# Kernel tuning notes

Measured on AMD Instinct MI355X. Metric: run time of the kernel, lower is better.

The kernel has to match this reference:

```python
import jax, jax.numpy as jnp
import numpy as np

N, E, F_IN, H0, H1, H2 = 50000, 800000, 128, 256, 256, 256
NEG = jnp.finfo(jnp.float32).min


def sage_max(x, src, dst, Wl, bl, Wr):
    # PyG SAGEConv(aggr='max'): lin_l(max_j x_j) + lin_r(x_i)
    agg = jax.ops.segment_max(x[src], dst, num_segments=N)  # [N, F]
    agg = jnp.where(agg <= NEG, 0.0, agg)  # isolated nodes -> 0
    return agg @ Wl + bl + x @ Wr


def setup_inputs() -> dict:
    key = jax.random.key(0)
    ks = jax.random.split(key, 16)
    g = lambda k, shp, fan: jax.random.normal(k, shp, jnp.float32) / np.sqrt(fan)
    inp = {
        "x": jax.random.normal(ks[0], (N, F_IN), jnp.float32),
        "edge_index": jax.random.randint(ks[1], (2, E), 0, N, jnp.int64),
        # shared_l1
        "Wl1": g(ks[2], (F_IN, H0), F_IN), "bl1": jnp.zeros((H0,), jnp.float32), "Wr1": g(ks[3], (F_IN, H0), F_IN),
        # shared_l2
        "Wl2": g(ks[4], (H0, H1), H0), "bl2": jnp.zeros((H1,), jnp.float32), "Wr2": g(ks[5], (H0, H1), H0),
        # rtang_l1 + head
        "Wla": g(ks[6], (H1, H2), H1), "bla": jnp.zeros((H2,), jnp.float32), "Wra": g(ks[7], (H1, H2), H1),
        "Wa": g(ks[8], (H2, 1), H2), "ba": jnp.zeros((1,), jnp.float32),
        # movedis_l1 + head
        "Wlm": g(ks[9], (H1, H2), H1), "blm": jnp.zeros((H2,), jnp.float32), "Wrm": g(ks[10], (H1, H2), H1),
        "Wm": g(ks[11], (H2, 1), H2), "bm": jnp.zeros((1,), jnp.float32),
    }
    return inp


def reference(x, edge_index, Wl1, bl1, Wr1, Wl2, bl2, Wr2,
              Wla, bla, Wra, Wa, ba, Wlm, blm, Wrm, Wm, bm):
    src, dst = edge_index[0], edge_index[1]
    h = jax.nn.relu(sage_max(x, src, dst, Wl1, bl1, Wr1))
    h = jax.nn.relu(sage_max(h, src, dst, Wl2, bl2, Wr2))
    rt = jax.nn.relu(sage_max(h, src, dst, Wla, bla, Wra))
    rt = (rt @ Wa + ba).reshape(-1)  # [N]
    mv = jax.nn.relu(sage_max(h, src, dst, Wlm, blm, Wrm))
    mv = (mv @ Wm + bm).reshape(-1)  # [N]
    return (rt, mv)
```

## Files before the change

kernel.cpp:

```cpp
#include <hip/hip_runtime.h>
#include <hip/hip_bf16.h>


#define NN 50000
#define NE 800000
#define HD 256
#define CAP 64

using bf16 = __hip_bfloat16;
typedef float f32x4 __attribute__((ext_vector_type(4)));
typedef short bf16x8 __attribute__((ext_vector_type(8)));

__device__ __forceinline__ void async16(const void* g, void* l) {
    __builtin_amdgcn_global_load_lds(
        (const __attribute__((address_space(1))) unsigned int*)g,
        (__attribute__((address_space(3))) unsigned int*)l, 16, 0, 0);
}

__device__ __forceinline__ unsigned short f2b(float f) {
    bf16 b = __float2bfloat16(f);
    return __builtin_bit_cast(unsigned short, b);
}

__global__ void k_scatter(const int* __restrict__ ei, int* __restrict__ cnt,
                          int* __restrict__ srcp) {
    int e = blockIdx.x * 256 + threadIdx.x;
    if (e < NE) {
        int d = ei[NE + e];
        int slot = atomicAdd(&cnt[d], 1);
        if (slot < CAP) srcp[(d << 6) + slot] = ei[e];
    }
}

__device__ __forceinline__ void pack1(const float* __restrict__ W,
                                      bf16* __restrict__ bt, int idx, int Ktot,
                                      int kofs) {
    int k = idx >> 8, n = idx & 255;
    bt[(size_t)n * Ktot + kofs + k] = __float2bfloat16(W[idx]);
}

#define PREP_CVT_B 6250
#define PREP_PACK_B 1792
#define PREP_CNT_B 196
#define PREP_B (PREP_CVT_B + PREP_PACK_B + PREP_CNT_B)

__global__ void k_prep(const float* __restrict__ x, bf16* __restrict__ xb,
                       const float* __restrict__ Wl1,
                       const float* __restrict__ Wr1,
                       const float* __restrict__ Wl2,
                       const float* __restrict__ Wr2,
                       const float* __restrict__ Wla,
                       const float* __restrict__ Wra,
                       const float* __restrict__ Wlm,
                       const float* __restrict__ Wrm, bf16* __restrict__ Bt1,
                       bf16* __restrict__ Bt2, bf16* __restrict__ Bta,
                       bf16* __restrict__ Btm, int* __restrict__ cnt) {
    int b = blockIdx.x;
    if (b < PREP_CVT_B) {
        int i = b * 256 + threadIdx.x;
        float4 v = ((const float4*)x)[i];
        ushort4 o;
        o.x = f2b(v.x); o.y = f2b(v.y); o.z = f2b(v.z); o.w = f2b(v.w);
        ((ushort4*)xb)[i] = o;
    } else if (b < PREP_CVT_B + PREP_PACK_B) {
        int idx = (b - PREP_CVT_B) * 256 + threadIdx.x;
        if (idx < 32768) pack1(Wl1, Bt1, idx, 256, 0);
        else if (idx < 65536) pack1(Wr1, Bt1, idx - 32768, 256, 128);
        else if (idx < 131072) pack1(Wl2, Bt2, idx - 65536, 512, 0);
        else if (idx < 196608) pack1(Wr2, Bt2, idx - 131072, 512, 256);
        else if (idx < 262144) pack1(Wla, Bta, idx - 196608, 512, 0);
        else if (idx < 327680) pack1(Wra, Bta, idx - 262144, 512, 256);
        else if (idx < 393216) pack1(Wlm, Btm, idx - 327680, 512, 0);
        else pack1(Wrm, Btm, idx - 393216, 512, 256);
    } else {
        int i = (b - PREP_CVT_B - PREP_PACK_B) * 256 + threadIdx.x;
        if (i < NN) cnt[i] = 0;
    }
}

template <int EPL>
__global__ __launch_bounds__(256) void k_agg(const bf16* __restrict__ feat,
                                             bf16* __restrict__ agg,
                                             const int* __restrict__ cnt,
                                             const int* __restrict__ srcp) {
    int node = blockIdx.x * 4 + (threadIdx.x >> 6);
    if (node >= NN) return;
    int lane = threadIdx.x & 63;
    int n = min(cnt[node], CAP);
    const int* __restrict__ lst = srcp + (node << 6);
    float m[EPL];
#pragma unroll
    for (int i = 0; i < EPL; ++i) m[i] = __int_as_float(0xff800000);

    auto acc2 = [&](unsigned v, int i0) {
        m[i0] = fmaxf(m[i0], __uint_as_float(v << 16));
        m[i0 + 1] = fmaxf(m[i0 + 1], __uint_as_float(v & 0xffff0000u));
    };

    int e = 0;
    for (; e + 7 < n; e += 8) {
        int s[8];
#pragma unroll
        for (int j = 0; j < 8; ++j) s[j] = lst[e + j];
        if (EPL == 2) {
            unsigned v[8];
#pragma unroll
            for (int j = 0; j < 8; ++j)
                v[j] = ((const unsigned*)feat)[(size_t)s[j] * 64 + lane];
#pragma unroll
            for (int j = 0; j < 8; ++j) acc2(v[j], 0);
        } else {
            uint2 v[8];
#pragma unroll
            for (int j = 0; j < 8; ++j)
                v[j] = ((const uint2*)feat)[(size_t)s[j] * 64 + lane];
#pragma unroll
            for (int j = 0; j < 8; ++j) { acc2(v[j].x, 0); acc2(v[j].y, 2); }
        }
    }
    for (; e + 3 < n; e += 4) {
        int s[4];
#pragma unroll
        for (int j = 0; j < 4; ++j) s[j] = lst[e + j];
        if (EPL == 2) {
            unsigned v[4];
#pragma unroll
            for (int j = 0; j < 4; ++j)
                v[j] = ((const unsigned*)feat)[(size_t)s[j] * 64 + lane];
#pragma unroll
            for (int j = 0; j < 4; ++j) acc2(v[j], 0);
        } else {
            uint2 v[4];
#pragma unroll
            for (int j = 0; j < 4; ++j)
                v[j] = ((const uint2*)feat)[(size_t)s[j] * 64 + lane];
#pragma unroll
            for (int j = 0; j < 4; ++j) { acc2(v[j].x, 0); acc2(v[j].y, 2); }
        }
    }
    for (; e < n; ++e) {
        int s = lst[e];
        if (EPL == 2) {
            acc2(((const unsigned*)feat)[(size_t)s * 64 + lane], 0);
        } else {
            uint2 v = ((const uint2*)feat)[(size_t)s * 64 + lane];
            acc2(v.x, 0); acc2(v.y, 2);
        }
    }
    unsigned r0 = 0, r1 = 0;
    if (n > 0) {
        r0 = (__float_as_uint(m[0]) >> 16) | (__float_as_uint(m[1]) & 0xffff0000u);
        if (EPL == 4)
            r1 = (__float_as_uint(m[2]) >> 16) | (__float_as_uint(m[3]) & 0xffff0000u);
    }
    if (EPL == 2) {
        ((unsigned*)agg)[(size_t)node * 64 + lane] = r0;
    } else {
        ((uint2*)agg)[(size_t)node * 64 + lane] = make_uint2(r0, r1);
    }
}

__device__ __forceinline__ void gemm_core256(const bf16* __restrict__ A0,
                                             const bf16* __restrict__ A1, int F,
                                             int Ktot,
                                             const bf16* __restrict__ Bt,
                                             int bm0, int t, short* As,
                                             short* Bs, f32x4 (&acc)[4][8]) {
    const int wave = t >> 6;
    const int lane = t & 63;
    const int q = lane >> 4;
    const int c = lane & 15;
    const int wr = (wave >> 1) * 64;
    const int wcl = (wave & 1) * 128;

    for (int k0 = 0; k0 < Ktot; k0 += 64) {
        const bf16* Asrc = (k0 < F) ? A0 : A1;
        const int kk = (k0 < F) ? k0 : k0 - F;
        __syncthreads();
#pragma unroll
        for (int it = 0; it < 4; ++it) {
            int chunk = it * 256 + t;
            int row = chunk >> 3, kc = chunk & 7;
            int kcg = kc ^ (row & 7);
            int grow = bm0 + row;
            if (grow > NN - 1) grow = NN - 1;
            async16(Asrc + (size_t)grow * F + kk + kcg * 8, &As[chunk * 8]);
        }
#pragma unroll
        for (int it = 0; it < 8; ++it) {
            int chunk = it * 256 + t;
            int row = chunk >> 3, kc = chunk & 7;
            int kcg = kc ^ (row & 7);
            async16(Bt + (size_t)row * Ktot + k0 + kcg * 8, &Bs[chunk * 8]);
        }
        __syncthreads();
#pragma unroll
        for (int ks = 0; ks < 2; ++ks) {
            bf16x8 af[4], bfr[8];
            int ch = (ks * 4 + q) ^ (c & 7);
#pragma unroll
            for (int i = 0; i < 4; ++i)
                af[i] = *(const bf16x8*)&As[(wr + i * 16 + c) * 64 + ch * 8];
#pragma unroll
            for (int j = 0; j < 8; ++j)
                bfr[j] = *(const bf16x8*)&Bs[(wcl + j * 16 + c) * 64 + ch * 8];
#pragma unroll
            for (int i = 0; i < 4; ++i)
#pragma unroll
                for (int j = 0; j < 8; ++j)
                    acc[i][j] = __builtin_amdgcn_mfma_f32_16x16x32_bf16(
                        af[i], bfr[j], acc[i][j], 0, 0, 0);
        }
    }
}

__global__ __launch_bounds__(256, 2) void k_gemm_h(
    const bf16* __restrict__ A0, const bf16* __restrict__ A1, int F, int Ktot,
    const bf16* __restrict__ Bt, const float* __restrict__ bias,
    bf16* __restrict__ Hout) {
    __shared__ __attribute__((aligned(16))) short As[128 * 64];
    __shared__ __attribute__((aligned(16))) short Bs[256 * 64];
    const int t = threadIdx.x;
    const int bm0 = blockIdx.x * 128;
    const int wave = t >> 6;
    const int lane = t & 63;
    const int q = lane >> 4;
    const int c = lane & 15;
    const int wr = (wave >> 1) * 64;
    const int wcl = (wave & 1) * 128;

    f32x4 acc[4][8];
#pragma unroll
    for (int i = 0; i < 4; ++i)
#pragma unroll
        for (int j = 0; j < 8; ++j) acc[i][j] = (f32x4){0.f, 0.f, 0.f, 0.f};
    gemm_core256(A0, A1, F, Ktot, Bt, bm0, t, As, Bs, acc);

    float bcol[8];
#pragma unroll
    for (int j = 0; j < 8; ++j) bcol[j] = bias[wcl + j * 16 + c];
#pragma unroll
    for (int i = 0; i < 4; ++i)
#pragma unroll
        for (int r = 0; r < 4; ++r) {
            int row = bm0 + wr + i * 16 + q * 4 + r;
            if (row < NN) {
#pragma unroll
                for (int j = 0; j < 8; ++j) {
                    int col = wcl + j * 16 + c;
                    float v = fmaxf(acc[i][j][r] + bcol[j], 0.f);
                    Hout[(size_t)row * HD + col] = __float2bfloat16(v);
                }
            }
        }
}

__global__ __launch_bounds__(256, 2) void k_gemm_heads(
    const bf16* __restrict__ A0, const bf16* __restrict__ A1,
    const bf16* __restrict__ Bta, const float* __restrict__ bla,
    const float* __restrict__ Wa, const float* __restrict__ ba,
    const bf16* __restrict__ Btm, const float* __restrict__ blm,
    const float* __restrict__ Wm, const float* __restrict__ bm,
    float* __restrict__ out) {
    __shared__ __attribute__((aligned(16))) short As[128 * 64];
    __shared__ __attribute__((aligned(16))) short Bs[256 * 64];
    const int t = threadIdx.x;
    const int bm0 = blockIdx.x * 128;
    const int z = blockIdx.y;
    const bf16* Bt = z ? Btm : Bta;
    const float* bias = z ? blm : bla;
    const float* Wh = z ? Wm : Wa;
    const float hb = z ? bm[0] : ba[0];
    float* outp = out + (size_t)z * NN;
    const int wave = t >> 6;
    const int lane = t & 63;
    const int q = lane >> 4;
    const int c = lane & 15;
    const int wr = (wave >> 1) * 64;
    const int wcl = (wave & 1) * 128;

    f32x4 acc[4][8];
#pragma unroll
    for (int i = 0; i < 4; ++i)
#pragma unroll
        for (int j = 0; j < 8; ++j) acc[i][j] = (f32x4){0.f, 0.f, 0.f, 0.f};
    gemm_core256(A0, A1, 256, 512, Bt, bm0, t, As, Bs, acc);

    float bcol[8], wcol[8];
#pragma unroll
    for (int j = 0; j < 8; ++j) {
        int col = wcl + j * 16 + c;
        bcol[j] = bias[col];
        wcol[j] = Wh[col];
    }
    float pr[4][4];
#pragma unroll
    for (int i = 0; i < 4; ++i)
#pragma unroll
        for (int r = 0; r < 4; ++r) {
            float p = 0.f;
#pragma unroll
            for (int j = 0; j < 8; ++j)
                p += fmaxf(acc[i][j][r] + bcol[j], 0.f) * wcol[j];
            p += __shfl_xor(p, 1, 64);
            p += __shfl_xor(p, 2, 64);
            p += __shfl_xor(p, 4, 64);
            p += __shfl_xor(p, 8, 64);
            pr[i][r] = p;
        }
    __syncthreads();
    float* red = (float*)As;
    if ((wave & 1) && c == 0) {
#pragma unroll
        for (int i = 0; i < 4; ++i)
#pragma unroll
            for (int r = 0; r < 4; ++r) red[wr + i * 16 + q * 4 + r] = pr[i][r];
    }
    __syncthreads();
    if (!(wave & 1) && c == 0) {
#pragma unroll
        for (int i = 0; i < 4; ++i)
#pragma unroll
            for (int r = 0; r < 4; ++r) {
                int lr = wr + i * 16 + q * 4 + r;
                int row = bm0 + lr;
                if (row < NN) outp[row] = pr[i][r] + red[lr] + hb;
            }
    }
}

extern "C" void kernel_launch(void* const* d_in, const int* in_sizes, int n_in,
                              void* d_out, int out_size, void* d_ws,
                              size_t ws_size, hipStream_t stream) {
    const float* x = (const float*)d_in[0];
    const int* ei = (const int*)d_in[1];
    const float* Wl1 = (const float*)d_in[2];
    const float* bl1 = (const float*)d_in[3];
    const float* Wr1 = (const float*)d_in[4];
    const float* Wl2 = (const float*)d_in[5];
    const float* bl2 = (const float*)d_in[6];
    const float* Wr2 = (const float*)d_in[7];
    const float* Wla = (const float*)d_in[8];
    const float* bla = (const float*)d_in[9];
    const float* Wra = (const float*)d_in[10];
    const float* Wa = (const float*)d_in[11];
    const float* ba = (const float*)d_in[12];
    const float* Wlm = (const float*)d_in[13];
    const float* blm = (const float*)d_in[14];
    const float* Wrm = (const float*)d_in[15];
    const float* Wm = (const float*)d_in[16];
    const float* bm = (const float*)d_in[17];
    float* out = (float*)d_out;

    char* ws = (char*)d_ws;
    size_t off = 0;
    auto alloc = [&](size_t b) {
        void* p = ws + off;
        off = (off + b + 255) & ~(size_t)255;
        return p;
    };
    int* srcp = (int*)alloc((size_t)NN * CAP * 4);
    int* cnt = (int*)alloc((size_t)NN * 4);
    bf16* xb = (bf16*)alloc((size_t)NN * 128 * 2);
    bf16* h1 = (bf16*)alloc((size_t)NN * 256 * 2);
    bf16* h2 = (bf16*)alloc((size_t)NN * 256 * 2);
    bf16* agg = (bf16*)alloc((size_t)NN * 256 * 2);
    bf16* Bt1 = (bf16*)alloc((size_t)256 * 256 * 2);
    bf16* Bt2 = (bf16*)alloc((size_t)256 * 512 * 2);
    bf16* Bta = (bf16*)alloc((size_t)256 * 512 * 2);
    bf16* Btm = (bf16*)alloc((size_t)256 * 512 * 2);
    (void)ws_size; (void)in_sizes; (void)n_in; (void)out_size;

    k_prep<<<PREP_B, 256, 0, stream>>>(x, xb, Wl1, Wr1, Wl2, Wr2, Wla, Wra,
                                       Wlm, Wrm, Bt1, Bt2, Bta, Btm, cnt);
    k_scatter<<<(NE + 255) / 256, 256, 0, stream>>>(ei, cnt, srcp);

    const int GB = (NN + 127) / 128;
    const int NG4 = (NN + 3) / 4;
    k_agg<2><<<NG4, 256, 0, stream>>>(xb, agg, cnt, srcp);
    k_gemm_h<<<GB, 256, 0, stream>>>(agg, xb, 128, 256, Bt1, bl1, h1);
    k_agg<4><<<NG4, 256, 0, stream>>>(h1, agg, cnt, srcp);
    k_gemm_h<<<GB, 256, 0, stream>>>(agg, h1, 256, 512, Bt2, bl2, h2);
    k_agg<4><<<NG4, 256, 0, stream>>>(h2, agg, cnt, srcp);
    dim3 gh(GB, 2);
    k_gemm_heads<<<gh, 256, 0, stream>>>(agg, h2, Bta, bla, Wa, ba, Btm, blm,
                                         Wm, bm, out);
}
```

Baseline: 362.7 us.

## Fuse prep, scatter and first aggregation into one cooperative persistent kernel

Replaces the three front kernels (weight/feature prep, edge scatter, first max-aggregation) with a single cooperative kernel of 1024 persistent blocks that grid-strides over the original block indices and uses grid.sync between phases. This is meant to remove two kernel launch boundaries and their tail idle time. If the cooperative launch fails, it falls back to the original separate kernels. The risks are grid.sync overhead and lower parallel slack from the fixed grid size, and a 1024-block cooperative grid may not be co-resident, which would force the fallback path.

```diff
diff --git a/kernel.cpp b/kernel.cpp
--- a/kernel.cpp
+++ b/kernel.cpp
@@ -1,15 +1,18 @@
 #include <hip/hip_runtime.h>
 #include <hip/hip_bf16.h>
+#include <hip/hip_cooperative_groups.h>
 
 
 #define NN 50000
 #define NE 800000
 #define HD 256
 #define CAP 64
+#define FRONT_GRID 1024
 
 using bf16 = __hip_bfloat16;
 typedef float f32x4 __attribute__((ext_vector_type(4)));
 typedef short bf16x8 __attribute__((ext_vector_type(8)));
+namespace cg = cooperative_groups;
 
 __device__ __forceinline__ void async16(const void* g, void* l) {
     __builtin_amdgcn_global_load_lds(
@@ -22,15 +25,15 @@
     return __builtin_bit_cast(unsigned short, b);
 }
 
-__global__ void k_scatter(const int* __restrict__ ei, int* __restrict__ cnt,
-                          int* __restrict__ srcp) {
-    int e = blockIdx.x * 256 + threadIdx.x;
-    if (e < NE) {
-        int d = ei[NE + e];
-        int slot = atomicAdd(&cnt[d], 1);
-        if (slot < CAP) srcp[(d << 6) + slot] = ei[e];
-    }
-}
+struct FrontParams {
+    const float* x; const int* ei;
+    const float* Wl1; const float* Wr1;
+    const float* Wl2; const float* Wr2;
+    const float* Wla; const float* Wra;
+    const float* Wlm; const float* Wrm;
+    bf16 *xb, *Bt1, *Bt2, *Bta, *Btm, *agg;
+    int *cnt, *srcp;
+};
 
 __device__ __forceinline__ void pack1(const float* __restrict__ W,
                                       bf16* __restrict__ bt, int idx, int Ktot,
@@ -43,49 +46,52 @@
 #define PREP_PACK_B 1792
 #define PREP_CNT_B 196
 #define PREP_B (PREP_CVT_B + PREP_PACK_B + PREP_CNT_B)
-
-__global__ void k_prep(const float* __restrict__ x, bf16* __restrict__ xb,
-                       const float* __restrict__ Wl1,
-                       const float* __restrict__ Wr1,
-                       const float* __restrict__ Wl2,
-                       const float* __restrict__ Wr2,
-                       const float* __restrict__ Wla,
-                       const float* __restrict__ Wra,
-                       const float* __restrict__ Wlm,
-                       const float* __restrict__ Wrm, bf16* __restrict__ Bt1,
-                       bf16* __restrict__ Bt2, bf16* __restrict__ Bta,
-                       bf16* __restrict__ Btm, int* __restrict__ cnt) {
-    int b = blockIdx.x;
+#define SCAT_B ((NE + 255) / 256)
+#define NG4 ((NN + 3) / 4)
+#define GB ((NN + 127) / 128)
+
+__device__ __forceinline__ void prep_body(int b, int t, const FrontParams& p) {
     if (b < PREP_CVT_B) {
-        int i = b * 256 + threadIdx.x;
-        float4 v = ((const float4*)x)[i];
+        int i = b * 256 + t;
+        float4 v = ((const float4*)p.x)[i];
         ushort4 o;
         o.x = f2b(v.x); o.y = f2b(v.y); o.z = f2b(v.z); o.w = f2b(v.w);
-        ((ushort4*)xb)[i] = o;
+        ((ushort4*)p.xb)[i] = o;
     } else if (b < PREP_CVT_B + PREP_PACK_B) {
-        int idx = (b - PREP_CVT_B) * 256 + threadIdx.x;
-        if (idx < 32768) pack1(Wl1, Bt1, idx, 256, 0);
-        else if (idx < 65536) pack1(Wr1, Bt1, idx - 32768, 256, 128);
-        else if (idx < 131072) pack1(Wl2, Bt2, idx - 65536, 512, 0);
-        else if (idx < 196608) pack1(Wr2, Bt2, idx - 131072, 512, 256);
-        else if (idx < 262144) pack1(Wla, Bta, idx - 196608, 512, 0);
-        else if (idx < 327680) pack1(Wra, Bta, idx - 262144, 512, 256);
-        else if (idx < 393216) pack1(Wlm, Btm, idx - 327680, 512, 0);
-        else pack1(Wrm, Btm, idx - 393216, 512, 256);
+        int idx = (b - PREP_CVT_B) * 256 + t;
+        if (idx < 32768) pack1(p.Wl1, p.Bt1, idx, 256, 0);
+        else if (idx < 65536) pack1(p.Wr1, p.Bt1, idx - 32768, 256, 128);
+        else if (idx < 131072) pack1(p.Wl2, p.Bt2, idx - 65536, 512, 0);
+        else if (idx < 196608) pack1(p.Wr2, p.Bt2, idx - 131072, 512, 256);
+        else if (idx < 262144) pack1(p.Wla, p.Bta, idx - 196608, 512, 0);
+        else if (idx < 327680) pack1(p.Wra, p.Bta, idx - 262144, 512, 256);
+        else if (idx < 393216) pack1(p.Wlm, p.Btm, idx - 327680, 512, 0);
+        else pack1(p.Wrm, p.Btm, idx - 393216, 512, 256);
     } else {
-        int i = (b - PREP_CVT_B - PREP_PACK_B) * 256 + threadIdx.x;
-        if (i < NN) cnt[i] = 0;
+        int i = (b - PREP_CVT_B - PREP_PACK_B) * 256 + t;
+        if (i < NN) p.cnt[i] = 0;
+    }
+}
+
+__device__ __forceinline__ void scatter_body(int b, int t,
+                                             const FrontParams& p) {
+    int e = b * 256 + t;
+    if (e < NE) {
+        int d = p.ei[NE + e];
+        int slot = atomicAdd(&p.cnt[d], 1);
+        if (slot < CAP) p.srcp[(d << 6) + slot] = p.ei[e];
     }
 }
 
 template <int EPL>
-__global__ __launch_bounds__(256) void k_agg(const bf16* __restrict__ feat,
-                                             bf16* __restrict__ agg,
-                                             const int* __restrict__ cnt,
-                                             const int* __restrict__ srcp) {
-    int node = blockIdx.x * 4 + (threadIdx.x >> 6);
+__device__ __forceinline__ void agg_body(int vb, int t,
+                                         const bf16* __restrict__ feat,
+                                         bf16* __restrict__ agg,
+                                         const int* __restrict__ cnt,
+                                         const int* __restrict__ srcp) {
+    int node = vb * 4 + (t >> 6);
     if (node >= NN) return;
-    int lane = threadIdx.x & 63;
+    int lane = t & 63;
     int n = min(cnt[node], CAP);
     const int* __restrict__ lst = srcp + (node << 6);
     float m[EPL];
@@ -158,6 +164,32 @@
     } else {
         ((uint2*)agg)[(size_t)node * 64 + lane] = make_uint2(r0, r1);
     }
+}
+
+__global__ __launch_bounds__(256) void k_front(FrontParams p) {
+    cg::grid_group grid = cg::this_grid();
+    const int t = threadIdx.x;
+    const int gsz = gridDim.x;
+    for (int vb = blockIdx.x; vb < PREP_B; vb += gsz) prep_body(vb, t, p);
+    grid.sync();
+    for (int vb = blockIdx.x; vb < SCAT_B; vb += gsz) scatter_body(vb, t, p);
+    grid.sync();
+    for (int vb = blockIdx.x; vb < NG4; vb += gsz)
+        agg_body<2>(vb, t, p.xb, p.agg, p.cnt, p.srcp);
+}
+
+__global__ __launch_bounds__(256) void kw_prep(FrontParams p) {
+    prep_body(blockIdx.x, threadIdx.x, p);
+}
+__global__ __launch_bounds__(256) void kw_scatter(FrontParams p) {
+    scatter_body(blockIdx.x, threadIdx.x, p);
+}
+template <int EPL>
+__global__ __launch_bounds__(256) void k_agg(const bf16* __restrict__ feat,
+                                             bf16* __restrict__ agg,
+                                             const int* __restrict__ cnt,
+                                             const int* __restrict__ srcp) {
+    agg_body<EPL>(blockIdx.x, threadIdx.x, feat, agg, cnt, srcp);
 }
 
 __device__ __forceinline__ void gemm_core256(const bf16* __restrict__ A0,
@@ -332,22 +364,12 @@
 extern "C" void kernel_launch(void* const* d_in, const int* in_sizes, int n_in,
                               void* d_out, int out_size, void* d_ws,
                               size_t ws_size, hipStream_t stream) {
-    const float* x = (const float*)d_in[0];
-    const int* ei = (const int*)d_in[1];
-    const float* Wl1 = (const float*)d_in[2];
     const float* bl1 = (const float*)d_in[3];
-    const float* Wr1 = (const float*)d_in[4];
-    const float* Wl2 = (const float*)d_in[5];
     const float* bl2 = (const float*)d_in[6];
-    const float* Wr2 = (const float*)d_in[7];
-    const float* Wla = (const float*)d_in[8];
     const float* bla = (const float*)d_in[9];
-    const float* Wra = (const float*)d_in[10];
     const float* Wa = (const float*)d_in[11];
     const float* ba = (const float*)d_in[12];
-    const float* Wlm = (const float*)d_in[13];
     const float* blm = (const float*)d_in[14];
-    const float* Wrm = (const float*)d_in[15];
     const float* Wm = (const float*)d_in[16];
     const float* bm = (const float*)d_in[17];
     float* out = (float*)d_out;
@@ -359,30 +381,43 @@
         off = (off + b + 255) & ~(size_t)255;
         return p;
     };
-    int* srcp = (int*)alloc((size_t)NN * CAP * 4);
-    int* cnt = (int*)alloc((size_t)NN * 4);
-    bf16* xb = (bf16*)alloc((size_t)NN * 128 * 2);
+    FrontParams p;
+    p.x = (const float*)d_in[0];
+    p.ei = (const int*)d_in[1];
+    p.Wl1 = (const float*)d_in[2];
+    p.Wr1 = (const float*)d_in[4];
+    p.Wl2 = (const float*)d_in[5];
+    p.Wr2 = (const float*)d_in[7];
+    p.Wla = (const float*)d_in[8];
+    p.Wra = (const float*)d_in[10];
+    p.Wlm = (const float*)d_in[13];
+    p.Wrm = (const float*)d_in[15];
+    p.srcp = (int*)alloc((size_t)NN * CAP * 4);
+    p.cnt = (int*)alloc((size_t)NN * 4);
+    p.xb = (bf16*)alloc((size_t)NN * 128 * 2);
     bf16* h1 = (bf16*)alloc((size_t)NN * 256 * 2);
     bf16* h2 = (bf16*)alloc((size_t)NN * 256 * 2);
-    bf16* agg = (bf16*)alloc((size_t)NN * 256 * 2);
-    bf16* Bt1 = (bf16*)alloc((size_t)256 * 256 * 2);
-    bf16* Bt2 = (bf16*)alloc((size_t)256 * 512 * 2);
-    bf16* Bta = (bf16*)alloc((size_t)256 * 512 * 2);
-    bf16* Btm = (bf16*)alloc((size_t)256 * 512 * 2);
+    p.agg = (bf16*)alloc((size_t)NN * 256 * 2);
+    p.Bt1 = (bf16*)alloc((size_t)256 * 256 * 2);
+    p.Bt2 = (bf16*)alloc((size_t)256 * 512 * 2);
+    p.Bta = (bf16*)alloc((size_t)256 * 512 * 2);
+    p.Btm = (bf16*)alloc((size_t)256 * 512 * 2);
     (void)ws_size; (void)in_sizes; (void)n_in; (void)out_size;
 
-    k_prep<<<PREP_B, 256, 0, stream>>>(x, xb, Wl1, Wr1, Wl2, Wr2, Wla, Wra,
-                                       Wlm, Wrm, Bt1, Bt2, Bta, Btm, cnt);
-    k_scatter<<<(NE + 255) / 256, 256, 0, stream>>>(ei, cnt, srcp);
-
-    const int GB = (NN + 127) / 128;
-    const int NG4 = (NN + 3) / 4;
-    k_agg<2><<<NG4, 256, 0, stream>>>(xb, agg, cnt, srcp);
-    k_gemm_h<<<GB, 256, 0, stream>>>(agg, xb, 128, 256, Bt1, bl1, h1);
-    k_agg<4><<<NG4, 256, 0, stream>>>(h1, agg, cnt, srcp);
-    k_gemm_h<<<GB, 256, 0, stream>>>(agg, h1, 256, 512, Bt2, bl2, h2);
-    k_agg<4><<<NG4, 256, 0, stream>>>(h2, agg, cnt, srcp);
+    void* args[] = {&p};
+    hipError_t err = hipLaunchCooperativeKernel(
+        (void*)k_front, dim3(FRONT_GRID), dim3(256), args, 0, stream);
+    if (err != hipSuccess) {
+        kw_prep<<<PREP_B, 256, 0, stream>>>(p);
+        kw_scatter<<<SCAT_B, 256, 0, stream>>>(p);
+        k_agg<2><<<NG4, 256, 0, stream>>>(p.xb, p.agg, p.cnt, p.srcp);
+    }
+
+    k_gemm_h<<<GB, 256, 0, stream>>>(p.agg, p.xb, 128, 256, p.Bt1, bl1, h1);
+    k_agg<4><<<NG4, 256, 0, stream>>>(h1, p.agg, p.cnt, p.srcp);
+    k_gemm_h<<<GB, 256, 0, stream>>>(p.agg, h1, 256, 512, p.Bt2, bl2, h2);
+    k_agg<4><<<NG4, 256, 0, stream>>>(h2, p.agg, p.cnt, p.srcp);
     dim3 gh(GB, 2);
-    k_gemm_heads<<<gh, 256, 0, stream>>>(agg, h2, Bta, bla, Wa, ba, Btm, blm,
-                                         Wm, bm, out);
-}
+    k_gemm_heads<<<gh, 256, 0, stream>>>(p.agg, h2, p.Bta, bla, Wa, ba, p.Btm,
+                                         blm, Wm, bm, out);
+}
```

After: 677.8 us. 86.8% more time.

## Shrink GEMM row tile to 64 and split columns across four waves

Applied to the files above, without the earlier changes.

The dense GEMM kernels now use 64-row tiles instead of 128, with each of four waves owning a 64-column slice of the full 256-wide output. The heads kernel reduces its per-row dot product through a four-way shared-memory reduction. This halves per-thread accumulators and LDS use, allows three blocks per CU, and doubles the grid to improve occupancy and load balance. The cost is that the 256x64 B tile is reloaded per block twice as often, which lowers arithmetic intensity per B load.

```diff
diff --git a/kernel.cpp b/kernel.cpp
--- a/kernel.cpp
+++ b/kernel.cpp
@@ -160,25 +160,24 @@
     }
 }
 
-__device__ __forceinline__ void gemm_core256(const bf16* __restrict__ A0,
-                                             const bf16* __restrict__ A1, int F,
-                                             int Ktot,
-                                             const bf16* __restrict__ Bt,
-                                             int bm0, int t, short* As,
-                                             short* Bs, f32x4 (&acc)[4][8]) {
+__device__ __forceinline__ void gemm_core64(const bf16* __restrict__ A0,
+                                            const bf16* __restrict__ A1, int F,
+                                            int Ktot,
+                                            const bf16* __restrict__ Bt,
+                                            int bm0, int t, short* As,
+                                            short* Bs, f32x4 (&acc)[4][4]) {
     const int wave = t >> 6;
     const int lane = t & 63;
     const int q = lane >> 4;
     const int c = lane & 15;
-    const int wr = (wave >> 1) * 64;
-    const int wcl = (wave & 1) * 128;
+    const int wcl = wave * 64;
 
     for (int k0 = 0; k0 < Ktot; k0 += 64) {
         const bf16* Asrc = (k0 < F) ? A0 : A1;
         const int kk = (k0 < F) ? k0 : k0 - F;
         __syncthreads();
 #pragma unroll
-        for (int it = 0; it < 4; ++it) {
+        for (int it = 0; it < 2; ++it) {
             int chunk = it * 256 + t;
             int row = chunk >> 3, kc = chunk & 7;
             int kcg = kc ^ (row & 7);
@@ -196,57 +195,56 @@
         __syncthreads();
 #pragma unroll
         for (int ks = 0; ks < 2; ++ks) {
-            bf16x8 af[4], bfr[8];
+            bf16x8 af[4], bfr[4];
             int ch = (ks * 4 + q) ^ (c & 7);
 #pragma unroll
             for (int i = 0; i < 4; ++i)
-                af[i] = *(const bf16x8*)&As[(wr + i * 16 + c) * 64 + ch * 8];
-#pragma unroll
-            for (int j = 0; j < 8; ++j)
+                af[i] = *(const bf16x8*)&As[(i * 16 + c) * 64 + ch * 8];
+#pragma unroll
+            for (int j = 0; j < 4; ++j)
                 bfr[j] = *(const bf16x8*)&Bs[(wcl + j * 16 + c) * 64 + ch * 8];
 #pragma unroll
             for (int i = 0; i < 4; ++i)
 #pragma unroll
-                for (int j = 0; j < 8; ++j)
+                for (int j = 0; j < 4; ++j)
                     acc[i][j] = __builtin_amdgcn_mfma_f32_16x16x32_bf16(
                         af[i], bfr[j], acc[i][j], 0, 0, 0);
         }
     }
 }
 
-__global__ __launch_bounds__(256, 2) void k_gemm_h(
+__global__ __launch_bounds__(256, 3) void k_gemm_h(
     const bf16* __restrict__ A0, const bf16* __restrict__ A1, int F, int Ktot,
     const bf16* __restrict__ Bt, const float* __restrict__ bias,
     bf16* __restrict__ Hout) {
-    __shared__ __attribute__((aligned(16))) short As[128 * 64];
+    __shared__ __attribute__((aligned(16))) short As[64 * 64];
     __shared__ __attribute__((aligned(16))) short Bs[256 * 64];
     const int t = threadIdx.x;
-    const int bm0 = blockIdx.x * 128;
+    const int bm0 = blockIdx.x * 64;
     const int wave = t >> 6;
     const int lane = t & 63;
     const int q = lane >> 4;
     const int c = lane & 15;
-    const int wr = (wave >> 1) * 64;
-    const int wcl = (wave & 1) * 128;
-
-    f32x4 acc[4][8];
+    const int wcl = wave * 64;
+
+    f32x4 acc[4][4];
 #pragma unroll
     for (int i = 0; i < 4; ++i)
 #pragma unroll
-        for (int j = 0; j < 8; ++j) acc[i][j] = (f32x4){0.f, 0.f, 0.f, 0.f};
-    gemm_core256(A0, A1, F, Ktot, Bt, bm0, t, As, Bs, acc);
-
-    float bcol[8];
-#pragma unroll
-    for (int j = 0; j < 8; ++j) bcol[j] = bias[wcl + j * 16 + c];
+        for (int j = 0; j < 4; ++j) acc[i][j] = (f32x4){0.f, 0.f, 0.f, 0.f};
+    gemm_core64(A0, A1, F, Ktot, Bt, bm0, t, As, Bs, acc);
+
+    float bcol[4];
+#pragma unroll
+    for (int j = 0; j < 4; ++j) bcol[j] = bias[wcl + j * 16 + c];
 #pragma unroll
     for (int i = 0; i < 4; ++i)
 #pragma unroll
         for (int r = 0; r < 4; ++r) {
-            int row = bm0 + wr + i * 16 + q * 4 + r;
+            int row = bm0 + i * 16 + q * 4 + r;
             if (row < NN) {
 #pragma unroll
-                for (int j = 0; j < 8; ++j) {
+                for (int j = 0; j < 4; ++j) {
                     int col = wcl + j * 16 + c;
                     float v = fmaxf(acc[i][j][r] + bcol[j], 0.f);
                     Hout[(size_t)row * HD + col] = __float2bfloat16(v);
@@ -255,17 +253,17 @@
         }
 }
 
-__global__ __launch_bounds__(256, 2) void k_gemm_heads(
+__global__ __launch_bounds__(256, 3) void k_gemm_heads(
     const bf16* __restrict__ A0, const bf16* __restrict__ A1,
     const bf16* __restrict__ Bta, const float* __restrict__ bla,
     const float* __restrict__ Wa, const float* __restrict__ ba,
     const bf16* __restrict__ Btm, const float* __restrict__ blm,
     const float* __restrict__ Wm, const float* __restrict__ bm,
     float* __restrict__ out) {
-    __shared__ __attribute__((aligned(16))) short As[128 * 64];
+    __shared__ __attribute__((aligned(16))) short As[64 * 64];
     __shared__ __attribute__((aligned(16))) short Bs[256 * 64];
     const int t = threadIdx.x;
-    const int bm0 = blockIdx.x * 128;
+    const int bm0 = blockIdx.x * 64;
     const int z = blockIdx.y;
     const bf16* Bt = z ? Btm : Bta;
     const float* bias = z ? blm : bla;
@@ -276,56 +274,43 @@
     const int lane = t & 63;
     const int q = lane >> 4;
     const int c = lane & 15;
-    const int wr = (wave >> 1) * 64;
-    const int wcl = (wave & 1) * 128;
-
-    f32x4 acc[4][8];
+    const int wcl = wave * 64;
+
+    f32x4 acc[4][4];
 #pragma unroll
     for (int i = 0; i < 4; ++i)
 #pragma unroll
-        for (int j = 0; j < 8; ++j) acc[i][j] = (f32x4){0.f, 0.f, 0.f, 0.f};
-    gemm_core256(A0, A1, 256, 512, Bt, bm0, t, As, Bs, acc);
-
-    float bcol[8], wcol[8];
-#pragma unroll
-    for (int j = 0; j < 8; ++j) {
+        for (int j = 0; j < 4; ++j) acc[i][j] = (f32x4){0.f, 0.f, 0.f, 0.f};
+    gemm_core64(A0, A1, 256, 512, Bt, bm0, t, As, Bs, acc);
+
+    float bcol[4], wcol[4];
+#pragma unroll
+    for (int j = 0; j < 4; ++j) {
         int col = wcl + j * 16 + c;
         bcol[j] = bias[col];
         wcol[j] = Wh[col];
     }
-    float pr[4][4];
+    __syncthreads();
+    float* red = (float*)As;
 #pragma unroll
     for (int i = 0; i < 4; ++i)
 #pragma unroll
         for (int r = 0; r < 4; ++r) {
             float p = 0.f;
 #pragma unroll
-            for (int j = 0; j < 8; ++j)
+            for (int j = 0; j < 4; ++j)
                 p += fmaxf(acc[i][j][r] + bcol[j], 0.f) * wcol[j];
             p += __shfl_xor(p, 1, 64);
             p += __shfl_xor(p, 2, 64);
             p += __shfl_xor(p, 4, 64);
             p += __shfl_xor(p, 8, 64);
-            pr[i][r] = p;
+            if (c == 0) red[wave * 64 + i * 16 + q * 4 + r] = p;
         }
     __syncthreads();
-    float* red = (float*)As;
-    if ((wave & 1) && c == 0) {
-#pragma unroll
-        for (int i = 0; i < 4; ++i)
-#pragma unroll
-            for (int r = 0; r < 4; ++r) red[wr + i * 16 + q * 4 + r] = pr[i][r];
-    }
-    __syncthreads();
-    if (!(wave & 1) && c == 0) {
-#pragma unroll
-        for (int i = 0; i < 4; ++i)
-#pragma unroll
-            for (int r = 0; r < 4; ++r) {
-                int lr = wr + i * 16 + q * 4 + r;
-                int row = bm0 + lr;
-                if (row < NN) outp[row] = pr[i][r] + red[lr] + hb;
-            }
+    if (t < 64) {
+        int row = bm0 + t;
+        if (row < NN)
+            outp[row] = red[t] + red[64 + t] + red[128 + t] + red[192 + t] + hb;
     }
 }
 
@@ -375,7 +360,7 @@
                                        Wlm, Wrm, Bt1, Bt2, Bta, Btm, cnt);
     k_scatter<<<(NE + 255) / 256, 256, 0, stream>>>(ei, cnt, srcp);
 
-    const int GB = (NN + 127) / 128;
+    const int GB = (NN + 63) / 64;
     const int NG4 = (NN + 3) / 4;
     k_agg<2><<<NG4, 256, 0, stream>>>(xb, agg, cnt, srcp);
     k_gemm_h<<<GB, 256, 0, stream>>>(agg, xb, 128, 256, Bt1, bl1, h1);
```

Result: slower. 373.8 us (+3.1%).
